# Performance work log

Hardware: AMD Instinct MI355X
Metric: run time of the kernel (lower is better)

## Reference

```python
import jax, jax.numpy as jnp
import numpy as np

B, S, H, NH, HD, V = 2, 2048, 1024, 16, 64, 32000
BASE = 10000.0
NEG = jnp.finfo(jnp.float32).min


def setup_inputs() -> dict:
    key = jax.random.key(0)
    ks = jax.random.split(key, 12)
    batch = jax.random.randint(ks[0], (B, S), 0, V)
    positions = jnp.broadcast_to(jnp.arange(S), (B, S))
    lengths = jax.random.randint(ks[1], (B,), 1, S + 1)  # >=1 to avoid fully-masked rows
    sc = 1.0 / np.sqrt(H)
    emb = jax.random.normal(ks[2], (V, H), dtype=jnp.float32) * 0.02
    wq = jax.random.normal(ks[3], (H, NH * HD), dtype=jnp.float32) * sc
    bq = jnp.zeros((NH * HD,), jnp.float32)
    wk = jax.random.normal(ks[4], (H, NH * HD), dtype=jnp.float32) * sc
    bk = jnp.zeros((NH * HD,), jnp.float32)
    wv = jax.random.normal(ks[5], (H, NH * HD), dtype=jnp.float32) * sc
    bv = jnp.zeros((NH * HD,), jnp.float32)
    wo = jax.random.normal(ks[6], (NH * HD, H), dtype=jnp.float32) * sc
    bo = jnp.zeros((H,), jnp.float32)
    return dict(batch=batch, positions=positions, lengths=lengths, emb=emb,
                wq=wq, bq=bq, wk=wk, bk=bk, wv=wv, bv=bv, wo=wo, bo=bo)


def _rope(x, positions):
    # x: [B, NH, S, HD]; positions: [B, S] int
    inv_freq = 1.0 / (BASE ** (jnp.arange(0, HD, 2, dtype=jnp.float32) / HD))  # [HD/2]
    freqs = positions.astype(jnp.float32)[..., None] * inv_freq               # [B, S, HD/2]
    ang = jnp.concatenate([freqs, freqs], axis=-1)                            # [B, S, HD]
    cos = jnp.cos(ang)[:, None]                                               # [B, 1, S, HD]
    sin = jnp.sin(ang)[:, None]
    x1, x2 = x[..., :HD // 2], x[..., HD // 2:]
    rot = jnp.concatenate([-x2, x1], axis=-1)
    return x * cos + rot * sin


def reference(batch, positions, lengths, emb, wq, bq, wk, bk, wv, bv, wo, bo):
    h = emb[batch]                                                 # [B, S, H]
    q = (h @ wq + bq).reshape(B, S, NH, HD).transpose(0, 2, 1, 3)  # [B, NH, S, HD]
    k = (h @ wk + bk).reshape(B, S, NH, HD).transpose(0, 2, 1, 3)
    v = (h @ wv + bv).reshape(B, S, NH, HD).transpose(0, 2, 1, 3)
    q = _rope(q, positions)
    k = _rope(k, positions)
    scores = jnp.einsum('bhqd,bhkd->bhqk', q, k) / np.sqrt(HD)     # [B, NH, S, S]
    causal = jnp.triu(jnp.full((S, S), NEG, jnp.float32), 1)
    pad = jnp.where(jnp.arange(S)[None, :] < lengths[:, None], 0.0, NEG)  # [B, S]
    mask = pad[:, None, None, :] + causal[None, None]              # [B, 1, S, S]
    attn = jax.nn.softmax(scores + mask, axis=-1)
    out = jnp.einsum('bhqk,bhkd->bhqd', attn, v)                   # [B, NH, S, HD]
    out = out.transpose(0, 2, 1, 3).reshape(B, S, NH * HD)
    return out @ wo + bo                                           # [B, S, H]
```

## Files before the change

### kernel.cpp

```cpp
#include <hip/hip_runtime.h>
#include <hip/hip_bf16.h>
#include <cstdint>

#define DEVINL __device__ __forceinline__

typedef __attribute__((ext_vector_type(8))) short short8;
typedef __attribute__((ext_vector_type(4))) short bhalf4;
typedef __attribute__((ext_vector_type(4))) float f32x4;

constexpr int B_ = 2, S_ = 2048, H_ = 1024, NH_ = 16, HD_ = 64;
constexpr int M_ = B_ * S_;
constexpr float SCALE = 0.125f;

DEVINL float bf2f(unsigned short h) {
    unsigned u = ((unsigned)h) << 16;
    float f; __builtin_memcpy(&f, &u, 4); return f;
}
DEVINL unsigned short f2bf(float f) {
    unsigned u; __builtin_memcpy(&u, &f, 4);
    u += 0x7FFFu + ((u >> 16) & 1u);
    return (unsigned short)(u >> 16);
}
DEVINL float ldin(const void* p, size_t i, int fp32) {
    return fp32 ? ((const float*)p)[i] : bf2f(((const unsigned short*)p)[i]);
}
DEVINL void gl16(const void* g, void* l) {
    __builtin_amdgcn_global_load_lds(
        (const __attribute__((address_space(1))) unsigned int*)g,
        (__attribute__((address_space(3))) unsigned int*)l, 16, 0, 0);
}
DEVINL f32x4 mfma16(short8 a, short8 b, f32x4 c) {
    return __builtin_amdgcn_mfma_f32_16x16x32_bf16(a, b, c, 0, 0, 0);
}
DEVINL void fsincos(float rev01, float* sn, float* cs) {
#if __has_builtin(__builtin_amdgcn_sinf) && __has_builtin(__builtin_amdgcn_cosf)
    *sn = __builtin_amdgcn_sinf(rev01);
    *cs = __builtin_amdgcn_cosf(rev01);
#else
    float a = rev01 * 6.28318530717958647692f;
    *sn = __sinf(a); *cs = __cosf(a);
#endif
}
DEVINL int detect_fp32(const unsigned short* emb, int t) {
    unsigned short hw = emb[2 * t];
    unsigned e = (hw >> 7) & 0xFFu;
    int s = (((e >= 90u) && (e <= 126u)) || ((hw & 0x7FFFu) == 0u)) ? 1 : 0;
    #pragma unroll
    for (int o = 1; o < 64; o <<= 1) s += __shfl_xor(s, o);
    __shared__ int cnt[4];
    if ((t & 63) == 0) cnt[t >> 6] = s;
    __syncthreads();
    return ((cnt[0] + cnt[1] + cnt[2] + cnt[3]) > 192) ? 0 : 1;
}

__global__ __launch_bounds__(256) void k_bias(const void* bq, const void* bk,
                                              const void* bv, const void* bo,
                                              const unsigned short* __restrict__ emb,
                                              int* __restrict__ flag,
                                              float* __restrict__ out) {
    int t = threadIdx.x;
    int fp32 = detect_fp32(emb, t);
    if (blockIdx.x == 0 && t == 0) flag[0] = fp32;
    int i = blockIdx.x * 256 + t;
    const void* src = (i < 1024) ? bq : (i < 2048) ? bk : (i < 3072) ? bv : bo;
    out[i] = ldin(src, (size_t)(i & 1023), fp32);
}

__global__ __launch_bounds__(256) void k_transw(const void* w0, const void* w1,
                                                const void* w2, const void* w3,
                                                const int* __restrict__ flag,
                                                unsigned short* __restrict__ wT) {
    __shared__ float tile[32][33];
    int mat = blockIdx.z;
    const void* w = (mat == 0) ? w0 : (mat == 1) ? w1 : (mat == 2) ? w2 : w3;
    int fp32 = flag[0];
    int n0 = blockIdx.x * 32, k0 = blockIdx.y * 32;
    int tx = threadIdx.x, ty = threadIdx.y;
    for (int i = ty; i < 32; i += 8)
        tile[i][tx] = ldin(w, (size_t)(k0 + i) * 1024 + n0 + tx, fp32);
    __syncthreads();
    unsigned short* dst = wT + (size_t)mat * 1024 * 1024;
    for (int i = ty; i < 32; i += 8)
        dst[(size_t)(n0 + i) * 1024 + k0 + tx] = f2bf(tile[tx][i]);
}

__global__ __launch_bounds__(256) void k_gather(const int* __restrict__ batch,
                                                const void* __restrict__ emb,
                                                const int* __restrict__ flag,
                                                unsigned short* __restrict__ h) {
    if (flag[0] == 0) return;
    int row = blockIdx.x, t = threadIdx.x;
    int tok = batch[row];
    const float4* s = (const float4*)((const float*)emb + (size_t)tok * H_);
    float4 x = s[t];
    unsigned long long pk = (unsigned long long)f2bf(x.x)
                          | ((unsigned long long)f2bf(x.y) << 16)
                          | ((unsigned long long)f2bf(x.z) << 32)
                          | ((unsigned long long)f2bf(x.w) << 48);
    ((unsigned long long*)(h + (size_t)row * H_))[t] = pk;
}

__global__ __launch_bounds__(256) void k_gemm_qkv(const unsigned short* __restrict__ embb,
                                                  const unsigned short* __restrict__ hbuf,
                                                  const int* __restrict__ batch,
                                                  const unsigned short* __restrict__ Bt,
                                                  const float* __restrict__ bias,
                                                  const int* __restrict__ positions,
                                                  const int* __restrict__ flag,
                                                  unsigned short* __restrict__ qo,
                                                  unsigned short* __restrict__ ko,
                                                  unsigned short* __restrict__ vt) {
    constexpr int K = 1024;
    __shared__ alignas(16) unsigned short As[2][128 * 32];
    __shared__ alignas(16) unsigned short Bs[2][128 * 32];
    int t = threadIdx.x, lane = t & 63, quad = lane >> 4, n16 = lane & 15;
    int w = t >> 6, wm = w >> 1, wn = w & 1;
    int m0 = blockIdx.y * 128, n0 = blockIdx.x * 128;
    int fp32 = flag[0];
    int r0 = t >> 2, r1 = 64 + r0;
    int ka = (t & 3) * 8;
    const unsigned short* a0;
    const unsigned short* a1;
    if (fp32) {
        a0 = hbuf + (size_t)(m0 + r0) * K;
        a1 = hbuf + (size_t)(m0 + r1) * K;
    } else {
        a0 = embb + (size_t)batch[m0 + r0] * K;
        a1 = embb + (size_t)batch[m0 + r1] * K;
    }
    const unsigned short* b0 = Bt + (size_t)(n0 + r0) * K;
    const unsigned short* b1 = Bt + (size_t)(n0 + r1) * K;
    f32x4 acc[4][4];
    #pragma unroll
    for (int mi = 0; mi < 4; mi++)
        #pragma unroll
        for (int ni = 0; ni < 4; ni++) acc[mi][ni] = (f32x4){0.f, 0.f, 0.f, 0.f};
    for (int k0 = 0; k0 < K; k0 += 64) {
        __syncthreads();
        gl16(a0 + k0 + ka,      &As[0][t * 8]);
        gl16(a1 + k0 + ka,      &As[0][(t + 256) * 8]);
        gl16(a0 + k0 + 32 + ka, &As[1][t * 8]);
        gl16(a1 + k0 + 32 + ka, &As[1][(t + 256) * 8]);
        gl16(b0 + k0 + ka,      &Bs[0][t * 8]);
        gl16(b1 + k0 + ka,      &Bs[0][(t + 256) * 8]);
        gl16(b0 + k0 + 32 + ka, &Bs[1][t * 8]);
        gl16(b1 + k0 + 32 + ka, &Bs[1][(t + 256) * 8]);
        __syncthreads();
        #pragma unroll
        for (int ks = 0; ks < 2; ks++) {
            short8 af[4], bfr[4];
            #pragma unroll
            for (int mi = 0; mi < 4; mi++)
                af[mi] = *(const short8*)&As[ks][(wm * 64 + mi * 16 + n16) * 32 + quad * 8];
            #pragma unroll
            for (int ni = 0; ni < 4; ni++)
                bfr[ni] = *(const short8*)&Bs[ks][(wn * 64 + ni * 16 + n16) * 32 + quad * 8];
            #pragma unroll
            for (int mi = 0; mi < 4; mi++)
                #pragma unroll
                for (int ni = 0; ni < 4; ni++)
                    acc[mi][ni] = mfma16(af[mi], bfr[ni], acc[mi][ni]);
        }
    }
    int colbase = n0 + wn * 64;
    int buf = colbase >> 10;
    int cc = colbase & 1023;
    float bb[4];
    #pragma unroll
    for (int ni = 0; ni < 4; ni++) bb[ni] = bias[colbase + ni * 16 + n16];
    if (buf == 2) {
        #pragma unroll
        for (int mi = 0; mi < 4; mi++) {
            int row = m0 + wm * 64 + mi * 16 + quad * 4;
            int bb_ = row >> 11, s0 = row & 2047;
            #pragma unroll
            for (int ni = 0; ni < 4; ni++) {
                int f = cc + ni * 16 + n16;
                unsigned long long pk = 0;
                #pragma unroll
                for (int i = 0; i < 4; i++)
                    pk |= (unsigned long long)f2bf(acc[mi][ni][i] + bb[ni]) << (16 * i);
                *(unsigned long long*)(vt + ((size_t)(bb_ * 1024 + f)) * 2048 + s0) = pk;
            }
        }
    } else {
        unsigned short* out = (buf == 0) ? qo : ko;
        float revf[2];
        #pragma unroll
        for (int ni = 0; ni < 2; ni++) {
            float d = (float)(ni * 16 + n16);
            revf[ni] = __expf(d * -0.28782313f) * 0.15915494f;
        }
        #pragma unroll
        for (int mi = 0; mi < 4; mi++) {
            int row0 = m0 + wm * 64 + mi * 16 + quad * 4;
            #pragma unroll
            for (int i = 0; i < 4; i++) {
                int row = row0 + i;
                float pos = (float)positions[row];
                #pragma unroll
                for (int ni = 0; ni < 2; ni++) {
                    float rev = pos * revf[ni];
                    float fr = rev - floorf(rev);
                    float sn, cs; fsincos(fr, &sn, &cs);
                    float x1 = acc[mi][ni][i] + bb[ni];
                    float x2 = acc[mi][ni + 2][i] + bb[ni + 2];
                    out[(size_t)row * 1024 + cc + ni * 16 + n16] = f2bf(x1 * cs - x2 * sn);
                    out[(size_t)row * 1024 + cc + (ni + 2) * 16 + n16] = f2bf(x2 * cs + x1 * sn);
                }
            }
        }
    }
}

__global__ __launch_bounds__(256) void k_attn(const unsigned short* __restrict__ q,
                                              const unsigned short* __restrict__ k_,
                                              const unsigned short* __restrict__ vt,
                                              const int* __restrict__ lengths,
                                              unsigned short* __restrict__ o) {
    __shared__ alignas(16) unsigned short Ks[64 * 64];
    __shared__ alignas(16) unsigned short Vs[64 * 64];
    int bx = blockIdx.x;
    int j = bx & 15, hh = (bx >> 4) & 15, b = bx >> 8;
    int t = threadIdx.x, w = t >> 6, lane = t & 63, quad = lane >> 4, n16 = lane & 15;
    int len = lengths[b];
    int tile0 = j, tile1 = 31 - j;
    int kend0 = min(tile0 * 64 + 64, len);
    int kend1 = min(tile1 * 64 + 64, len);
    int nkt = (kend1 + 63) >> 6;
    int qrow0 = tile0 * 64 + w * 16 + n16;
    int qrow1 = tile1 * 64 + w * 16 + n16;
    int limit0 = min(qrow0, len - 1);
    int limit1 = min(qrow1, len - 1);
    short8 qf[2][2];
    {
        size_t qa = ((size_t)(b * S_ + qrow0)) * H_ + hh * 64 + quad * 8;
        size_t qb2 = ((size_t)(b * S_ + qrow1)) * H_ + hh * 64 + quad * 8;
        qf[0][0] = *(const short8*)(q + qa);  qf[0][1] = *(const short8*)(q + qa + 32);
        qf[1][0] = *(const short8*)(q + qb2); qf[1][1] = *(const short8*)(q + qb2 + 32);
    }
    f32x4 oa[2][4];
    float m_[2], l_[2];
    #pragma unroll
    for (int s = 0; s < 2; s++) {
        m_[s] = -__builtin_inff(); l_[s] = 0.f;
        #pragma unroll
        for (int nb = 0; nb < 4; nb++) oa[s][nb] = (f32x4){0.f, 0.f, 0.f, 0.f};
    }
    int ky0 = t >> 3,        kc0 = (t & 7) ^ (ky0 & 7);
    int ky1 = (t + 256) >> 3, kc1 = (t & 7) ^ (ky1 & 7);
    const unsigned short* kbase = k_ + (size_t)b * S_ * H_ + hh * 64;
    const unsigned short* vbase = vt + ((size_t)(b * 1024 + hh * 64)) * 2048;
    for (int kt = 0; kt < nkt; kt++) {
        int kb = kt * 64;
        __syncthreads();
        gl16(kbase + (size_t)(kb + ky0) * H_ + kc0 * 8, &Ks[t * 8]);
        gl16(kbase + (size_t)(kb + ky1) * H_ + kc1 * 8, &Ks[(t + 256) * 8]);
        gl16(vbase + (size_t)ky0 * 2048 + kb + kc0 * 8, &Vs[t * 8]);
        gl16(vbase + (size_t)ky1 * 2048 + kb + kc1 * 8, &Vs[(t + 256) * 8]);
        __syncthreads();
        short8 kf[4][2];
        #pragma unroll
        for (int st = 0; st < 4; st++)
            #pragma unroll
            for (int hf = 0; hf < 2; hf++) {
                int ky = st * 16 + n16;
                int slot = ky * 8 + ((hf * 4 + quad) ^ (ky & 7));
                kf[st][hf] = *(const short8*)&Ks[slot * 8];
            }
        short8 vf8[2][4];
        #pragma unroll
        for (int p = 0; p < 2; p++)
            #pragma unroll
            for (int nb = 0; nb < 4; nb++) {
                int f = nb * 16 + n16;
                int cl0 = 4 * p + (quad >> 1);
                int cl1 = cl0 + 2;
                int off = (quad & 1) * 4;
                bhalf4 lo = *(const bhalf4*)&Vs[f * 64 + ((cl0 ^ (f & 7)) * 8 + off)];
                bhalf4 hi = *(const bhalf4*)&Vs[f * 64 + ((cl1 ^ (f & 7)) * 8 + off)];
                short8 cmb = {lo[0], lo[1], lo[2], lo[3], hi[0], hi[1], hi[2], hi[3]};
                vf8[p][nb] = cmb;
            }
        #pragma unroll
        for (int si = 0; si < 2; si++) {
            if (si == 0 && kb >= kend0) continue;
            int limit = si ? limit1 : limit0;
            f32x4 sc[4];
            #pragma unroll
            for (int st = 0; st < 4; st++) {
                f32x4 z = (f32x4){0.f, 0.f, 0.f, 0.f};
                z = mfma16(kf[st][0], qf[si][0], z);
                z = mfma16(kf[st][1], qf[si][1], z);
                sc[st] = z;
            }
            float mx = -__builtin_inff();
            #pragma unroll
            for (int st = 0; st < 4; st++)
                #pragma unroll
                for (int i = 0; i < 4; i++) {
                    int kg = kb + st * 16 + quad * 4 + i;
                    float val = sc[st][i] * SCALE;
                    val = (kg <= limit) ? val : -__builtin_inff();
                    sc[st][i] = val;
                    mx = fmaxf(mx, val);
                }
            mx = fmaxf(mx, __shfl_xor(mx, 16));
            mx = fmaxf(mx, __shfl_xor(mx, 32));
            float mnew = fmaxf(m_[si], mx);
            float alpha = __expf(m_[si] - mnew);
            m_[si] = mnew;
            float rs = 0.f;
            bhalf4 pf[4];
            #pragma unroll
            for (int st = 0; st < 4; st++)
                #pragma unroll
                for (int i = 0; i < 4; i++) {
                    float p = __expf(sc[st][i] - mnew);
                    rs += p;
                    pf[st][i] = (short)f2bf(p);
                }
            rs += __shfl_xor(rs, 16);
            rs += __shfl_xor(rs, 32);
            l_[si] = alpha * l_[si] + rs;
            f32x4 av;
            #pragma unroll
            for (int i = 0; i < 4; i++) av[i] = __shfl(alpha, quad * 4 + i);
            #pragma unroll
            for (int nb = 0; nb < 4; nb++) oa[si][nb] *= av;
            #pragma unroll
            for (int p = 0; p < 2; p++) {
                short8 pp = {pf[2 * p][0], pf[2 * p][1], pf[2 * p][2], pf[2 * p][3],
                             pf[2 * p + 1][0], pf[2 * p + 1][1], pf[2 * p + 1][2], pf[2 * p + 1][3]};
                #pragma unroll
                for (int nb = 0; nb < 4; nb++)
                    oa[si][nb] = mfma16(pp, vf8[p][nb], oa[si][nb]);
            }
        }
    }
    #pragma unroll
    for (int si = 0; si < 2; si++) {
        int tb = si ? tile1 : tile0;
        f32x4 rl;
        #pragma unroll
        for (int i = 0; i < 4; i++) rl[i] = 1.f / __shfl(l_[si], quad * 4 + i);
        #pragma unroll
        for (int nb = 0; nb < 4; nb++) {
            #pragma unroll
            for (int i = 0; i < 4; i++) {
                int row = tb * 64 + w * 16 + quad * 4 + i;
                o[((size_t)(b * S_ + row)) * H_ + hh * 64 + nb * 16 + n16] =
                    f2bf(oa[si][nb][i] * rl[i]);
            }
        }
    }
}

__global__ __launch_bounds__(256) void k_gemm64(const unsigned short* __restrict__ A,
                                                const unsigned short* __restrict__ Bt,
                                                const float* __restrict__ bias,
                                                unsigned short* __restrict__ Cb,
                                                float* __restrict__ Cf,
                                                const int* __restrict__ flag) {
    constexpr int K = 1024, N = 1024;
    __shared__ alignas(16) unsigned short As[2][64 * 32];
    __shared__ alignas(16) unsigned short Bs[2][128 * 32];
    int t = threadIdx.x, lane = t & 63, quad = lane >> 4, n16 = lane & 15;
    int w = t >> 6, wm = w & 1, wn = w >> 1;
    int m0 = blockIdx.y * 64, n0 = blockIdx.x * 128;
    int r0 = t >> 2, r1 = 64 + r0, ka = (t & 3) * 8;
    const unsigned short* a0 = A + (size_t)(m0 + r0) * K;
    const unsigned short* b0 = Bt + (size_t)(n0 + r0) * K;
    const unsigned short* b1 = Bt + (size_t)(n0 + r1) * K;
    f32x4 acc[2][4];
    #pragma unroll
    for (int mi = 0; mi < 2; mi++)
        #pragma unroll
        for (int ni = 0; ni < 4; ni++) acc[mi][ni] = (f32x4){0.f, 0.f, 0.f, 0.f};
    for (int k0 = 0; k0 < K; k0 += 64) {
        __syncthreads();
        gl16(a0 + k0 + ka,      &As[0][t * 8]);
        gl16(a0 + k0 + 32 + ka, &As[1][t * 8]);
        gl16(b0 + k0 + ka,      &Bs[0][t * 8]);
        gl16(b1 + k0 + ka,      &Bs[0][(t + 256) * 8]);
        gl16(b0 + k0 + 32 + ka, &Bs[1][t * 8]);
        gl16(b1 + k0 + 32 + ka, &Bs[1][(t + 256) * 8]);
        __syncthreads();
        #pragma unroll
        for (int ks = 0; ks < 2; ks++) {
            short8 af[2], bfr[4];
            #pragma unroll
            for (int mi = 0; mi < 2; mi++)
                af[mi] = *(const short8*)&As[ks][(wm * 32 + mi * 16 + n16) * 32 + quad * 8];
            #pragma unroll
            for (int ni = 0; ni < 4; ni++)
                bfr[ni] = *(const short8*)&Bs[ks][(wn * 64 + ni * 16 + n16) * 32 + quad * 8];
            #pragma unroll
            for (int mi = 0; mi < 2; mi++)
                #pragma unroll
                for (int ni = 0; ni < 4; ni++)
                    acc[mi][ni] = mfma16(af[mi], bfr[ni], acc[mi][ni]);
        }
    }
    int fp32out = (flag[0] == 1);
    #pragma unroll
    for (int mi = 0; mi < 2; mi++) {
        #pragma unroll
        for (int ni = 0; ni < 4; ni++) {
            int row = m0 + wm * 32 + mi * 16 + quad * 4;
            int col = n0 + wn * 64 + ni * 16 + n16;
            float bb = bias[col];
            #pragma unroll
            for (int i = 0; i < 4; i++) {
                float val = acc[mi][ni][i] + bb;
                size_t idx = (size_t)(row + i) * N + col;
                if (fp32out) Cf[idx] = val;
                else         Cb[idx] = f2bf(val);
            }
        }
    }
}

extern "C" void kernel_launch(void* const* d_in, const int* in_sizes, int n_in,
                              void* d_out, int out_size, void* d_ws, size_t ws_size,
                              hipStream_t stream) {
    (void)in_sizes; (void)n_in; (void)out_size; (void)ws_size;
    const int* batch     = (const int*)d_in[0];
    const int* positions = (const int*)d_in[1];
    const int* lengths   = (const int*)d_in[2];
    const void* emb = d_in[3];
    const void* wq = d_in[4];  const void* bq = d_in[5];
    const void* wk = d_in[6];  const void* bk = d_in[7];
    const void* wv = d_in[8];  const void* bv = d_in[9];
    const void* wo = d_in[10]; const void* bo = d_in[11];

    char* ws = (char*)d_ws;
    int*   flag   = (int*)ws;
    float* biasws = (float*)(ws + 4096);
    unsigned short* wT = (unsigned short*)(ws + 20480);
    size_t off = 20480 + (8ull << 20);
    unsigned short* hbuf = (unsigned short*)(ws + off); off += (8ull << 20);
    unsigned short* qb   = (unsigned short*)(ws + off); off += (8ull << 20);
    unsigned short* kb2  = (unsigned short*)(ws + off); off += (8ull << 20);
    unsigned short* vtb  = (unsigned short*)(ws + off); off += (8ull << 20);
    unsigned short* ao   = (unsigned short*)(ws + off); off += (8ull << 20);

    k_bias<<<16, 256, 0, stream>>>(bq, bk, bv, bo, (const unsigned short*)emb,
                                   flag, biasws);
    k_transw<<<dim3(32, 32, 4), dim3(32, 8), 0, stream>>>(wq, wk, wv, wo, flag, wT);
    k_gather<<<M_, 256, 0, stream>>>(batch, emb, flag, hbuf);

    k_gemm_qkv<<<dim3(3072 / 128, M_ / 128), 256, 0, stream>>>(
        (const unsigned short*)emb, hbuf, batch, wT, biasws, positions, flag,
        qb, kb2, vtb);

    k_attn<<<B_ * NH_ * 16, 256, 0, stream>>>(qb, kb2, vtb, lengths, ao);

    k_gemm64<<<dim3(1024 / 128, M_ / 64), 256, 0, stream>>>(
        ao, wT + (3ull << 20), biasws + 3072,
        (unsigned short*)d_out, (float*)d_out, flag);
}
```

Measured before the change: 320.1 us.

## Load attention K/V fragments directly from global and fold bias into transpose kernel

The attention kernel no longer stages K and V tiles through shared memory with two barriers per tile. Each lane now loads its MFMA fragments straight from global memory, which removes the LDS round trip and the syncs but sends more uncoalesced global traffic through L2. Separately, the bias-conversion and dtype-detect kernel is merged into the weight-transpose kernel to save one launch. In exchange, every transpose block now runs the fp32 detection on the embedding data.

```diff
diff --git a/kernel.cpp b/kernel.cpp
--- a/kernel.cpp
+++ b/kernel.cpp
@@ -53,29 +53,28 @@
     return ((cnt[0] + cnt[1] + cnt[2] + cnt[3]) > 192) ? 0 : 1;
 }
 
-__global__ __launch_bounds__(256) void k_bias(const void* bq, const void* bk,
-                                              const void* bv, const void* bo,
-                                              const unsigned short* __restrict__ emb,
-                                              int* __restrict__ flag,
-                                              float* __restrict__ out) {
-    int t = threadIdx.x;
-    int fp32 = detect_fp32(emb, t);
-    if (blockIdx.x == 0 && t == 0) flag[0] = fp32;
-    int i = blockIdx.x * 256 + t;
-    const void* src = (i < 1024) ? bq : (i < 2048) ? bk : (i < 3072) ? bv : bo;
-    out[i] = ldin(src, (size_t)(i & 1023), fp32);
-}
-
 __global__ __launch_bounds__(256) void k_transw(const void* w0, const void* w1,
                                                 const void* w2, const void* w3,
-                                                const int* __restrict__ flag,
+                                                const void* bq, const void* bk,
+                                                const void* bv, const void* bo,
+                                                const unsigned short* __restrict__ emb,
+                                                int* __restrict__ flag,
+                                                float* __restrict__ biasws,
                                                 unsigned short* __restrict__ wT) {
     __shared__ float tile[32][33];
+    int tx = threadIdx.x, ty = threadIdx.y, t = ty * 32 + tx;
+    int fp32 = detect_fp32(emb, t);
     int mat = blockIdx.z;
+    if (mat == 0 && blockIdx.y == 0) {
+        if (blockIdx.x == 0 && t == 0) flag[0] = fp32;
+        if (blockIdx.x < 16) {
+            int i = blockIdx.x * 256 + t;
+            const void* src = (i < 1024) ? bq : (i < 2048) ? bk : (i < 3072) ? bv : bo;
+            biasws[i] = ldin(src, (size_t)(i & 1023), fp32);
+        }
+    }
     const void* w = (mat == 0) ? w0 : (mat == 1) ? w1 : (mat == 2) ? w2 : w3;
-    int fp32 = flag[0];
     int n0 = blockIdx.x * 32, k0 = blockIdx.y * 32;
-    int tx = threadIdx.x, ty = threadIdx.y;
     for (int i = ty; i < 32; i += 8)
         tile[i][tx] = ldin(w, (size_t)(k0 + i) * 1024 + n0 + tx, fp32);
     __syncthreads();
@@ -218,8 +217,6 @@
                                               const unsigned short* __restrict__ vt,
                                               const int* __restrict__ lengths,
                                               unsigned short* __restrict__ o) {
-    __shared__ alignas(16) unsigned short Ks[64 * 64];
-    __shared__ alignas(16) unsigned short Vs[64 * 64];
     int bx = blockIdx.x;
     int j = bx & 15, hh = (bx >> 4) & 15, b = bx >> 8;
     int t = threadIdx.x, w = t >> 6, lane = t & 63, quad = lane >> 4, n16 = lane & 15;
@@ -247,40 +244,26 @@
         #pragma unroll
         for (int nb = 0; nb < 4; nb++) oa[s][nb] = (f32x4){0.f, 0.f, 0.f, 0.f};
     }
-    int ky0 = t >> 3,        kc0 = (t & 7) ^ (ky0 & 7);
-    int ky1 = (t + 256) >> 3, kc1 = (t & 7) ^ (ky1 & 7);
-    const unsigned short* kbase = k_ + (size_t)b * S_ * H_ + hh * 64;
-    const unsigned short* vbase = vt + ((size_t)(b * 1024 + hh * 64)) * 2048;
+    const unsigned short* kbase = k_ + ((size_t)b * S_) * H_ + hh * 64 + quad * 8;
+    const unsigned short* vbase = vt + ((size_t)(b * 1024 + hh * 64 + n16)) * 2048 + quad * 4;
     for (int kt = 0; kt < nkt; kt++) {
         int kb = kt * 64;
-        __syncthreads();
-        gl16(kbase + (size_t)(kb + ky0) * H_ + kc0 * 8, &Ks[t * 8]);
-        gl16(kbase + (size_t)(kb + ky1) * H_ + kc1 * 8, &Ks[(t + 256) * 8]);
-        gl16(vbase + (size_t)ky0 * 2048 + kb + kc0 * 8, &Vs[t * 8]);
-        gl16(vbase + (size_t)ky1 * 2048 + kb + kc1 * 8, &Vs[(t + 256) * 8]);
-        __syncthreads();
         short8 kf[4][2];
         #pragma unroll
-        for (int st = 0; st < 4; st++)
-            #pragma unroll
-            for (int hf = 0; hf < 2; hf++) {
-                int ky = st * 16 + n16;
-                int slot = ky * 8 + ((hf * 4 + quad) ^ (ky & 7));
-                kf[st][hf] = *(const short8*)&Ks[slot * 8];
-            }
-        short8 vf8[2][4];
+        for (int st = 0; st < 4; st++) {
+            const unsigned short* kr = kbase + (size_t)(kb + st * 16 + n16) * H_;
+            kf[st][0] = *(const short8*)kr;
+            kf[st][1] = *(const short8*)(kr + 32);
+        }
+        union U8 { unsigned long long u[2]; short8 v; };
+        U8 vf[2][4];
         #pragma unroll
         for (int p = 0; p < 2; p++)
             #pragma unroll
             for (int nb = 0; nb < 4; nb++) {
-                int f = nb * 16 + n16;
-                int cl0 = 4 * p + (quad >> 1);
-                int cl1 = cl0 + 2;
-                int off = (quad & 1) * 4;
-                bhalf4 lo = *(const bhalf4*)&Vs[f * 64 + ((cl0 ^ (f & 7)) * 8 + off)];
-                bhalf4 hi = *(const bhalf4*)&Vs[f * 64 + ((cl1 ^ (f & 7)) * 8 + off)];
-                short8 cmb = {lo[0], lo[1], lo[2], lo[3], hi[0], hi[1], hi[2], hi[3]};
-                vf8[p][nb] = cmb;
+                const unsigned short* vr = vbase + (size_t)(nb * 16) * 2048 + kb + 32 * p;
+                vf[p][nb].u[0] = *(const unsigned long long*)vr;
+                vf[p][nb].u[1] = *(const unsigned long long*)(vr + 16);
             }
         #pragma unroll
         for (int si = 0; si < 2; si++) {
@@ -334,7 +317,7 @@
                              pf[2 * p + 1][0], pf[2 * p + 1][1], pf[2 * p + 1][2], pf[2 * p + 1][3]};
                 #pragma unroll
                 for (int nb = 0; nb < 4; nb++)
-                    oa[si][nb] = mfma16(pp, vf8[p][nb], oa[si][nb]);
+                    oa[si][nb] = mfma16(pp, vf[p][nb].v, oa[si][nb]);
             }
         }
     }
@@ -445,9 +428,9 @@
     unsigned short* vtb  = (unsigned short*)(ws + off); off += (8ull << 20);
     unsigned short* ao   = (unsigned short*)(ws + off); off += (8ull << 20);
 
-    k_bias<<<16, 256, 0, stream>>>(bq, bk, bv, bo, (const unsigned short*)emb,
-                                   flag, biasws);
-    k_transw<<<dim3(32, 32, 4), dim3(32, 8), 0, stream>>>(wq, wk, wv, wo, flag, wT);
+    k_transw<<<dim3(32, 32, 4), dim3(32, 8), 0, stream>>>(
+        wq, wk, wv, wo, bq, bk, bv, bo, (const unsigned short*)emb,
+        flag, biasws, wT);
     k_gather<<<M_, 256, 0, stream>>>(batch, emb, flag, hbuf);
 
     k_gemm_qkv<<<dim3(3072 / 128, M_ / 128), 256, 0, stream>>>(
```

Result: slower. 380.2 us (+18.8%).
